# Optimization experiments

Hardware: AMD Instinct MI355X
Metric: run time of the kernel (lower is better)

Reference implementation:

```python
import jax, jax.numpy as jnp
import numpy as np

N_NODES = 50000
N_EDGES = 200000
D = 128
LN_EPS = 1e-5


def _layer_norm(x, g, b):
    mu = jnp.mean(x, axis=-1, keepdims=True)
    var = jnp.mean(jnp.square(x - mu), axis=-1, keepdims=True)
    return (x - mu) * jax.lax.rsqrt(var + LN_EPS) * g + b


def _mlp(x, W1, b1, W2, b2, W3, b3, g, beta):
    # 2 hidden ReLU layers + linear output + LayerNorm (MeshGraphNets style)
    h = jax.nn.relu(x @ W1 + b1)
    h = jax.nn.relu(h @ W2 + b2)
    h = h @ W3 + b3
    return _layer_norm(h, g, beta)


def setup_inputs() -> dict:
    key = jax.random.key(0)
    ks = jax.random.split(key, 12)
    d = {}
    d["node_features"] = jax.random.normal(ks[0], (N_NODES, D), dtype=jnp.float32)
    d["edge_features"] = jax.random.normal(ks[1], (N_EDGES, D), dtype=jnp.float32)
    d["senders"] = jax.random.randint(ks[2], (N_EDGES,), 0, N_NODES, dtype=jnp.int32)
    d["receivers"] = jax.random.randint(ks[3], (N_EDGES,), 0, N_NODES, dtype=jnp.int32)
    def lin(k, fan_in, fan_out):
        return jax.random.normal(k, (fan_in, fan_out), dtype=jnp.float32) / np.sqrt(fan_in)
    # edge MLP: [3D] -> D -> D -> D
    d["We1"] = lin(ks[4], 3 * D, D); d["be1"] = jnp.zeros((D,), jnp.float32)
    d["We2"] = lin(ks[5], D, D);     d["be2"] = jnp.zeros((D,), jnp.float32)
    d["We3"] = lin(ks[6], D, D);     d["be3"] = jnp.zeros((D,), jnp.float32)
    d["ge"] = jnp.ones((D,), jnp.float32); d["bege"] = jnp.zeros((D,), jnp.float32)
    # node MLP: [2D] -> D -> D -> D
    d["Wn1"] = lin(ks[7], 2 * D, D); d["bn1"] = jnp.zeros((D,), jnp.float32)
    d["Wn2"] = lin(ks[8], D, D);     d["bn2"] = jnp.zeros((D,), jnp.float32)
    d["Wn3"] = lin(ks[9], D, D);     d["bn3"] = jnp.zeros((D,), jnp.float32)
    d["gn"] = jnp.ones((D,), jnp.float32); d["begn"] = jnp.zeros((D,), jnp.float32)
    return d


def reference(node_features, edge_features, senders, receivers,
              We1, be1, We2, be2, We3, be3, ge, bege,
              Wn1, bn1, Wn2, bn2, Wn3, bn3, gn, begn):
    num_nodes = node_features.shape[0]
    # --- edge update: gather sender/receiver feats, concat, edge MLP ---
    edge_in = jnp.concatenate(
        [node_features[senders], node_features[receivers], edge_features], axis=-1)  # [E, 3D]
    new_edge = _mlp(edge_in, We1, be1, We2, be2, We3, be3, ge, bege)  # [E, D]
    # --- node update: scatter-sum aggregate, concat, node MLP ---
    agg = jax.ops.segment_sum(new_edge, receivers, num_segments=num_nodes)  # [N, D]
    node_in = jnp.concatenate([node_features, agg], axis=-1)  # [N, 2D]
    new_node = _mlp(node_in, Wn1, bn1, Wn2, bn2, Wn3, bn3, gn, begn)
    # --- residuals ---
    new_node = new_node + node_features
    new_edge = new_edge + edge_features
    return new_node, new_edge
```

## Files before the change

kernel.cpp:

```cpp
#include <hip/hip_runtime.h>

#define NNODES 50000
#define NEDGES 200000
#define DD 128
#define LN_EPS 1e-5f
#define NTH 256

typedef __attribute__((ext_vector_type(8))) short bf16x8;
typedef __attribute__((ext_vector_type(4))) float f32x4;
typedef __attribute__((ext_vector_type(16))) float f32x16;

template<int N> struct ic { static constexpr int value = N; };

__device__ __forceinline__ unsigned short bfr(float f) {
    union { float f; unsigned u; } v; v.f = f;
    return (unsigned short)((v.u + 0x7fffu + ((v.u >> 16) & 1u)) >> 16);
}
__device__ __forceinline__ unsigned pk2(float a, float b) {
    return (unsigned)bfr(a) | ((unsigned)bfr(b) << 16);
}
__device__ __forceinline__ void gload_lds16(const void* g, void* l) {
    __builtin_amdgcn_global_load_lds(
        (const __attribute__((address_space(1))) void*)g,
        (__attribute__((address_space(3))) void*)l, 16, 0, 0);
}

__global__ void build_wimg(const float* __restrict__ We1, const float* __restrict__ We2,
                           const float* __restrict__ We3, const float* __restrict__ Wn1,
                           const float* __restrict__ Wn2, const float* __restrict__ Wn3,
                           char* __restrict__ img_e, char* __restrict__ img_n) {
    int tid = blockIdx.x * NTH + threadIdx.x;
    const float* W; char* dst; int q;
    if      (tid <  6144) { W = We1; dst = img_e;             q = tid;         }
    else if (tid <  8192) { W = We2; dst = img_e + 12 * 8192; q = tid - 6144;  }
    else if (tid < 10240) { W = We3; dst = img_e + 16 * 8192; q = tid - 8192;  }
    else if (tid < 14336) { W = Wn1; dst = img_n;             q = tid - 10240; }
    else if (tid < 16384) { W = Wn2; dst = img_n + 8 * 8192;  q = tid - 14336; }
    else if (tid < 18432) { W = Wn3; dst = img_n + 12 * 8192; q = tid - 16384; }
    else return;
    int c = q >> 9, rem = q & 511;
    int nt = rem >> 7, r2 = rem & 127, n32 = r2 >> 2, ks = r2 & 3;
    int n = nt * 32 + n32;
    int sx = (n32 + (n32 >> 2)) & 3;
    int k0 = c * 32 + ks * 8;
    unsigned short o[8];
    #pragma unroll
    for (int e = 0; e < 8; ++e)
        o[e] = bfr(W[(size_t)(k0 + e) * DD + n]);
    uint4 val;
    val.x = (unsigned)o[0] | ((unsigned)o[1] << 16);
    val.y = (unsigned)o[2] | ((unsigned)o[3] << 16);
    val.z = (unsigned)o[4] | ((unsigned)o[5] << 16);
    val.w = (unsigned)o[6] | ((unsigned)o[7] << 16);
    *(uint4*)(dst + (size_t)c * 8192 + nt * 2048 + n32 * 64 + ((ks ^ sx) << 4)) = val;
}

__global__ __launch_bounds__(NTH)
void cvt_histo(const float* __restrict__ nodef, const int* __restrict__ recv,
               uint4* __restrict__ nodb, int* __restrict__ cnt) {
    const int tid0 = blockIdx.x * NTH + threadIdx.x;
    if (tid0 < NEDGES) atomicAdd(&cnt[recv[tid0]], 1);
    const int NG = NNODES * 16;
    for (int g = tid0; g < NG; g += gridDim.x * NTH) {
        f32x4 a = ((const f32x4*)nodef)[g * 2];
        f32x4 b = ((const f32x4*)nodef)[g * 2 + 1];
        uint4 o;
        o.x = pk2(a[0], a[1]); o.y = pk2(a[2], a[3]);
        o.z = pk2(b[0], b[1]); o.w = pk2(b[2], b[3]);
        nodb[g] = o;
    }
}

__global__ __launch_bounds__(NTH)
void csr_scan1(const int* __restrict__ cnt, int* __restrict__ part) {
    __shared__ int red[NTH];
    const int b = blockIdx.x, t = threadIdx.x;
    const int base = b * 196;
    int s = 0;
    for (int i = t; i < 196; i += NTH) {
        int idx = base + i;
        if (idx < NNODES) s += cnt[idx];
    }
    red[t] = s;
    __syncthreads();
    for (int d = NTH / 2; d > 0; d >>= 1) {
        if (t < d) red[t] += red[t + d];
        __syncthreads();
    }
    if (t == 0) part[b] = red[0];
}

__global__ __launch_bounds__(NTH)
void csr_scan2(const int* __restrict__ cnt, const int* __restrict__ part,
               int* __restrict__ off, int* __restrict__ cursor) {
    __shared__ int sp[NTH];
    const int t = threadIdx.x;
    sp[t] = part[t];
    __syncthreads();
    for (int d = 1; d < NTH; d <<= 1) {
        int v = (t >= d) ? sp[t - d] : 0;
        __syncthreads();
        sp[t] += v;
        __syncthreads();
    }
    int run = (t == 0) ? 0 : sp[t - 1];
    const int base = t * 196;
    for (int i = 0; i < 196; ++i) {
        int idx = base + i;
        if (idx < NNODES) { off[idx] = run; cursor[idx] = run; run += cnt[idx]; }
    }
    if (t == NTH - 1) off[NNODES] = NEDGES;
}

__global__ void csr_fill(const int* __restrict__ recv, int* __restrict__ cursor,
                         int* __restrict__ elist) {
    int e = blockIdx.x * NTH + threadIdx.x;
    if (e < NEDGES) {
        int p = atomicAdd(&cursor[recv[e]], 1);
        elist[p] = e;
    }
}

__global__ __launch_bounds__(NTH)
void aggregate(const unsigned* __restrict__ ybuf,
               const int* __restrict__ off, const int* __restrict__ elist,
               unsigned* __restrict__ aggb) {
    const int n = blockIdx.x * 4 + (threadIdx.x >> 6);
    const int l = threadIdx.x & 63;
    if (n >= NNODES) return;
    const int j0 = off[n], j1 = off[n + 1];
    float sx = 0.f, sy = 0.f;
    int j = j0;
    for (; j + 4 <= j1; j += 4) {
        unsigned v0 = ybuf[(size_t)elist[j] * 64 + l];
        unsigned v1 = ybuf[(size_t)elist[j + 1] * 64 + l];
        unsigned v2 = ybuf[(size_t)elist[j + 2] * 64 + l];
        unsigned v3 = ybuf[(size_t)elist[j + 3] * 64 + l];
        sx += __uint_as_float(v0 << 16) + __uint_as_float(v1 << 16)
            + __uint_as_float(v2 << 16) + __uint_as_float(v3 << 16);
        sy += __uint_as_float(v0 & 0xffff0000u) + __uint_as_float(v1 & 0xffff0000u)
            + __uint_as_float(v2 & 0xffff0000u) + __uint_as_float(v3 & 0xffff0000u);
    }
    for (; j < j1; ++j) {
        unsigned v = ybuf[(size_t)elist[j] * 64 + l];
        sx += __uint_as_float(v << 16);
        sy += __uint_as_float(v & 0xffff0000u);
    }
    aggb[(size_t)n * 64 + l] = pk2(sx, sy);
}

template<int MODE>
__global__ __launch_bounds__(NTH, 2)
void mgn_mfma(const float* __restrict__ nodef, const float* __restrict__ edgef,
              const unsigned short* __restrict__ nodb,
              const int* __restrict__ senders, const int* __restrict__ receivers,
              const char* __restrict__ img,
              const float* __restrict__ b1, const float* __restrict__ b2,
              const float* __restrict__ b3,
              const float* __restrict__ gamma, const float* __restrict__ beta,
              const unsigned short* __restrict__ aggb, unsigned* __restrict__ ybuf,
              float* __restrict__ outp)
{
    __shared__ char Wbuf[5 * 8192];
    __shared__ char Hb[4 * 8192];

    const int t  = threadIdx.x;
    const int w  = t >> 6;
    const int l  = t & 63;
    const int ln = l & 31;
    const int hi = l >> 5;
    const int row0 = blockIdx.x * 128;
    const int gm = row0 + w * 32 + ln;
    constexpr int NROWS = (MODE == 0) ? NEDGES : NNODES;
    constexpr int NK1   = (MODE == 0) ? 12 : 8;
    constexpr int NCH   = NK1 + 8;
    const int gmc = gm < NROWS ? gm : NROWS - 1;
    const int sxA = (ln + (ln >> 2)) & 3;
    const int sxH = ln & 15;

    int srow = 0, rrow = 0;
    if (MODE == 0) { srow = senders[gmc]; rrow = receivers[gmc]; }

    const f32x16 fz = {0.f,0.f,0.f,0.f,0.f,0.f,0.f,0.f,
                       0.f,0.f,0.f,0.f,0.f,0.f,0.f,0.f};
    f32x16 acc[4];
    #pragma unroll
    for (int nt = 0; nt < 4; ++nt) acc[nt] = fz;

    bf16x8 bS[3][2];
    f32x4  fS[3][4];

    auto stageW = [&](int c) {
        const char* src = img + (size_t)c * 8192 + t * 16;
        char* dstl = Wbuf + (c % 5) * 8192 + t * 16;
        gload_lds16(src, dstl);
        gload_lds16(src + 4096, dstl + 4096);
    };

    auto loadBB = [&](auto CC, bf16x8* dst) {
        constexpr int c = decltype(CC)::value;
        const unsigned short* base;
        if constexpr (MODE == 0) {
            base = (c < 4) ? nodb + (size_t)srow * DD : nodb + (size_t)rrow * DD;
        } else {
            base = (c < 4) ? nodb + (size_t)gmc * DD : aggb + (size_t)gmc * DD;
        }
        const char* p = (const char*)base + (c & 3) * 64 + hi * 16;
        dst[0] = *(const bf16x8*)p;
        dst[1] = *(const bf16x8*)(p + 32);
    };

    auto loadBF = [&](auto CC, f32x4* dst) {
        constexpr int c = decltype(CC)::value;
        const float* p = edgef + (size_t)gmc * DD + (c & 3) * 32 + hi * 8;
        dst[0] = *(const f32x4*)p;
        dst[1] = *(const f32x4*)(p + 4);
        dst[2] = *(const f32x4*)(p + 16);
        dst[3] = *(const f32x4*)(p + 20);
    };

    auto cvtB = [&](const f32x4* br) {
        union { unsigned u[4]; bf16x8 v; } r;
        r.u[0] = pk2(br[0][0], br[0][1]);
        r.u[1] = pk2(br[0][2], br[0][3]);
        r.u[2] = pk2(br[1][0], br[1][1]);
        r.u[3] = pk2(br[1][2], br[1][3]);
        return r.v;
    };

    auto loadBH = [&](int ks, int kh) {
        const char* p = Hb + w * 8192 + ln * 256
                      + (((ks * 4 + kh * 2 + hi) ^ sxH) << 4);
        return *(const bf16x8*)p;
    };

    auto getB = [&](auto CC, int kh) -> bf16x8 {
        constexpr int c = decltype(CC)::value;
        if constexpr (c >= NK1) {
            return loadBH((c - NK1) & 3, kh);
        } else if constexpr (MODE == 0 && c >= 8) {
            return cvtB(&fS[c % 3][kh * 2]);
        } else {
            return bS[c % 3][kh];
        }
    };

    auto compute = [&](auto CC) {
        constexpr int c = decltype(CC)::value;
        const char* bp = Wbuf + (c % 5) * 8192 + ln * 64;
        #pragma unroll
        for (int kh = 0; kh < 2; ++kh) {
            bf16x8 b = getB(CC, kh);
            #pragma unroll
            for (int nt = 0; nt < 4; ++nt) {
                bf16x8 a = *(const bf16x8*)(bp + nt * 2048
                            + (((kh * 2 + hi) ^ sxA) << 4));
                acc[nt] = __builtin_amdgcn_mfma_f32_32x32x16_bf16(a, b, acc[nt], 0, 0, 0);
            }
        }
    };

    auto epiH = [&](const float* bias) {
        #pragma unroll
        for (int nt = 0; nt < 4; ++nt) {
            #pragma unroll
            for (int rq = 0; rq < 4; ++rq) {
                f32x4 bv = *(const f32x4*)(bias + nt * 32 + rq * 8 + hi * 4);
                unsigned short h[4];
                #pragma unroll
                for (int j = 0; j < 4; ++j)
                    h[j] = bfr(fmaxf(acc[nt][rq * 4 + j] + bv[j], 0.f));
                char* p = Hb + w * 8192 + ln * 256
                        + (((nt * 4 + rq) ^ sxH) << 4) + hi * 8;
                unsigned lo = (unsigned)h[0] | ((unsigned)h[1] << 16);
                unsigned hx = (unsigned)h[2] | ((unsigned)h[3] << 16);
                *(unsigned long long*)p =
                    (unsigned long long)lo | ((unsigned long long)hx << 32);
            }
            acc[nt] = fz;
        }
    };

#define PITER(C, VM)                                                          \
    {                                                                         \
        if constexpr ((C) + 3 < NCH) stageW((C) + 3);                         \
        __builtin_amdgcn_sched_barrier(0);                                    \
        if constexpr ((C) + 2 < NK1) {                                        \
            if constexpr (MODE == 0 && (C) + 2 >= 8)                          \
                loadBF(ic<(C) + 2>{}, fS[((C) + 2) % 3]);                     \
            else                                                              \
                loadBB(ic<(C) + 2>{}, bS[((C) + 2) % 3]);                     \
        }                                                                     \
        __builtin_amdgcn_sched_barrier(0);                                    \
        asm volatile("s_waitcnt vmcnt(" #VM ")" ::: "memory");                \
        __builtin_amdgcn_sched_barrier(0);                                    \
        __builtin_amdgcn_s_barrier();                                         \
        __builtin_amdgcn_sched_barrier(0);                                    \
        compute(ic<(C)>{});                                                   \
    }

    stageW(0);
    __builtin_amdgcn_sched_barrier(0);
    loadBB(ic<0>{}, bS[0]);
    __builtin_amdgcn_sched_barrier(0);
    stageW(1);
    __builtin_amdgcn_sched_barrier(0);
    loadBB(ic<1>{}, bS[1]);
    __builtin_amdgcn_sched_barrier(0);
    stageW(2);
    __builtin_amdgcn_sched_barrier(0);

    if constexpr (MODE == 0) {
        PITER(0, 10)  PITER(1, 10)  PITER(2, 10)  PITER(3, 12)
        PITER(4, 12)  PITER(5, 12)  PITER(6, 14)  PITER(7, 16)
        PITER(8, 18)  PITER(9, 20)  PITER(10, 16) PITER(11, 12)
        epiH(b1);
        PITER(12, 8)  PITER(13, 4)  PITER(14, 4)  PITER(15, 4)
        epiH(b2);
        PITER(16, 4)  PITER(17, 2)  PITER(18, 0)  PITER(19, 0)
    } else {
        PITER(0, 10)  PITER(1, 10)  PITER(2, 10)  PITER(3, 12)
        PITER(4, 12)  PITER(5, 12)  PITER(6, 10)  PITER(7, 8)
        epiH(b1);
        PITER(8, 6)   PITER(9, 4)   PITER(10, 4)  PITER(11, 4)
        epiH(b2);
        PITER(12, 4)  PITER(13, 2)  PITER(14, 0)  PITER(15, 0)
    }
#undef PITER

    float vsum = 0.f, vsq = 0.f;
    #pragma unroll
    for (int nt = 0; nt < 4; ++nt) {
        #pragma unroll
        for (int rq = 0; rq < 4; ++rq) {
            f32x4 bv = *(const f32x4*)(b3 + nt * 32 + rq * 8 + hi * 4);
            #pragma unroll
            for (int j = 0; j < 4; ++j) {
                float v = acc[nt][rq * 4 + j] + bv[j];
                acc[nt][rq * 4 + j] = v;
                vsum += v; vsq += v * v;
            }
        }
    }
    vsum += __shfl_xor(vsum, 32);
    vsq  += __shfl_xor(vsq, 32);
    const float mu = vsum * (1.f / DD);
    const float rs = rsqrtf(vsq * (1.f / DD) - mu * mu + LN_EPS);

    if (gm < NROWS) {
        const float* resid = ((MODE == 0) ? edgef : nodef) + (size_t)gm * DD;
        #pragma unroll
        for (int nt = 0; nt < 4; ++nt) {
            #pragma unroll
            for (int rq = 0; rq < 4; ++rq) {
                const int n0 = nt * 32 + rq * 8 + hi * 4;
                f32x4 gv = *(const f32x4*)(gamma + n0);
                f32x4 bv = *(const f32x4*)(beta + n0);
                f32x4 rv = *(const f32x4*)(resid + n0);
                float y[4];
                f32x4 o;
                #pragma unroll
                for (int j = 0; j < 4; ++j) {
                    y[j] = (acc[nt][rq * 4 + j] - mu) * rs * gv[j] + bv[j];
                    o[j] = y[j] + rv[j];
                }
                *(f32x4*)(outp + (size_t)gm * DD + n0) = o;
                if (MODE == 0) {
                    unsigned long long pkd =
                        (unsigned long long)pk2(y[0], y[1])
                      | ((unsigned long long)pk2(y[2], y[3]) << 32);
                    *(unsigned long long*)((char*)ybuf + (size_t)gm * 256 + n0 * 2) = pkd;
                }
            }
        }
    }
}

extern "C" void kernel_launch(void* const* d_in, const int* in_sizes, int n_in,
                              void* d_out, int out_size, void* d_ws, size_t ws_size,
                              hipStream_t stream) {
    const float* nodef = (const float*)d_in[0];
    const float* edgef = (const float*)d_in[1];
    const int* senders   = (const int*)d_in[2];
    const int* receivers = (const int*)d_in[3];
    const float* We1 = (const float*)d_in[4],  *be1 = (const float*)d_in[5];
    const float* We2 = (const float*)d_in[6],  *be2 = (const float*)d_in[7];
    const float* We3 = (const float*)d_in[8],  *be3 = (const float*)d_in[9];
    const float* ge  = (const float*)d_in[10], *bege = (const float*)d_in[11];
    const float* Wn1 = (const float*)d_in[12], *bn1 = (const float*)d_in[13];
    const float* Wn2 = (const float*)d_in[14], *bn2 = (const float*)d_in[15];
    const float* Wn3 = (const float*)d_in[16], *bn3 = (const float*)d_in[17];
    const float* gn  = (const float*)d_in[18], *begn = (const float*)d_in[19];

    float* out_node = (float*)d_out;
    float* out_edge = (float*)d_out + (size_t)NNODES * DD;

    char* ws = (char*)d_ws;
    size_t o = 0;
    unsigned short* aggb = (unsigned short*)(ws + o); o += (size_t)NNODES * 256;
    unsigned* ybuf = (unsigned*)(ws + o);             o += (size_t)NEDGES * 256;
    unsigned short* nodb = (unsigned short*)(ws + o); o += (size_t)NNODES * 256;
    char* img_e = ws + o;           o += 20 * 8192;
    char* img_n = ws + o;           o += 16 * 8192;
    int* cnt    = (int*)(ws + o);   o += NNODES * 4;
    int* cursor = (int*)(ws + o);   o += NNODES * 4;
    int* off    = (int*)(ws + o);   o += (NNODES + 4) * 4;
    int* part   = (int*)(ws + o);   o += NTH * 4;
    int* elist  = (int*)(ws + o);   o += NEDGES * 4;

    hipMemsetAsync(cnt, 0, NNODES * 4, stream);
    cvt_histo<<<1024, NTH, 0, stream>>>(nodef, receivers, (uint4*)nodb, cnt);
    build_wimg<<<72, NTH, 0, stream>>>(We1, We2, We3, Wn1, Wn2, Wn3, img_e, img_n);
    csr_scan1<<<NTH, NTH, 0, stream>>>(cnt, part);
    csr_scan2<<<1, NTH, 0, stream>>>(cnt, part, off, cursor);
    csr_fill<<<(NEDGES + NTH - 1) / NTH, NTH, 0, stream>>>(receivers, cursor, elist);

    mgn_mfma<0><<<dim3((NEDGES + 127) / 128), dim3(NTH), 0, stream>>>(
        nodef, edgef, nodb, senders, receivers, img_e,
        be1, be2, be3, ge, bege, aggb, ybuf, out_edge);

    aggregate<<<(NNODES + 3) / 4, NTH, 0, stream>>>(ybuf, off, elist, (unsigned*)aggb);

    mgn_mfma<1><<<dim3((NNODES + 127) / 128), dim3(NTH), 0, stream>>>(
        nodef, edgef, nodb, senders, receivers, img_n,
        bn1, bn2, bn3, gn, begn, aggb, ybuf, out_node);
}
```

Before: 321.3 us.

## Scatter bf16 edge outputs into receiver-sorted order so aggregation reads contiguously

The CSR fill now records each edge's slot position (perm) rather than a list of edge ids. The edge MLP kernel writes its bf16 copy of each edge result directly into that receiver-sorted slot, so the aggregate kernel reads contiguous rows without the elist indirection. This trades a gathered read in aggregation for scattered 8-byte writes in the edge kernel. The PITER scheduling constants are also retuned.

```diff
diff --git a/kernel.cpp b/kernel.cpp
--- a/kernel.cpp
+++ b/kernel.cpp
@@ -113,17 +113,17 @@
 }
 
 __global__ void csr_fill(const int* __restrict__ recv, int* __restrict__ cursor,
-                         int* __restrict__ elist) {
+                         int* __restrict__ perm) {
     int e = blockIdx.x * NTH + threadIdx.x;
     if (e < NEDGES) {
         int p = atomicAdd(&cursor[recv[e]], 1);
-        elist[p] = e;
+        perm[e] = p;
     }
 }
 
 __global__ __launch_bounds__(NTH)
 void aggregate(const unsigned* __restrict__ ybuf,
-               const int* __restrict__ off, const int* __restrict__ elist,
+               const int* __restrict__ off,
                unsigned* __restrict__ aggb) {
     const int n = blockIdx.x * 4 + (threadIdx.x >> 6);
     const int l = threadIdx.x & 63;
@@ -132,17 +132,17 @@
     float sx = 0.f, sy = 0.f;
     int j = j0;
     for (; j + 4 <= j1; j += 4) {
-        unsigned v0 = ybuf[(size_t)elist[j] * 64 + l];
-        unsigned v1 = ybuf[(size_t)elist[j + 1] * 64 + l];
-        unsigned v2 = ybuf[(size_t)elist[j + 2] * 64 + l];
-        unsigned v3 = ybuf[(size_t)elist[j + 3] * 64 + l];
+        unsigned v0 = ybuf[(size_t)j * 64 + l];
+        unsigned v1 = ybuf[(size_t)(j + 1) * 64 + l];
+        unsigned v2 = ybuf[(size_t)(j + 2) * 64 + l];
+        unsigned v3 = ybuf[(size_t)(j + 3) * 64 + l];
         sx += __uint_as_float(v0 << 16) + __uint_as_float(v1 << 16)
             + __uint_as_float(v2 << 16) + __uint_as_float(v3 << 16);
         sy += __uint_as_float(v0 & 0xffff0000u) + __uint_as_float(v1 & 0xffff0000u)
             + __uint_as_float(v2 & 0xffff0000u) + __uint_as_float(v3 & 0xffff0000u);
     }
     for (; j < j1; ++j) {
-        unsigned v = ybuf[(size_t)elist[j] * 64 + l];
+        unsigned v = ybuf[(size_t)j * 64 + l];
         sx += __uint_as_float(v << 16);
         sy += __uint_as_float(v & 0xffff0000u);
     }
@@ -154,6 +154,7 @@
 void mgn_mfma(const float* __restrict__ nodef, const float* __restrict__ edgef,
               const unsigned short* __restrict__ nodb,
               const int* __restrict__ senders, const int* __restrict__ receivers,
+              const int* __restrict__ perm,
               const char* __restrict__ img,
               const float* __restrict__ b1, const float* __restrict__ b2,
               const float* __restrict__ b3,
@@ -178,8 +179,8 @@
     const int sxA = (ln + (ln >> 2)) & 3;
     const int sxH = ln & 15;
 
-    int srow = 0, rrow = 0;
-    if (MODE == 0) { srow = senders[gmc]; rrow = receivers[gmc]; }
+    int srow = 0, rrow = 0, prow = 0;
+    if (MODE == 0) { srow = senders[gmc]; rrow = receivers[gmc]; prow = perm[gmc]; }
 
     const f32x16 fz = {0.f,0.f,0.f,0.f,0.f,0.f,0.f,0.f,
                        0.f,0.f,0.f,0.f,0.f,0.f,0.f,0.f};
@@ -311,20 +312,20 @@
     __builtin_amdgcn_sched_barrier(0);
 
     if constexpr (MODE == 0) {
-        PITER(0, 10)  PITER(1, 10)  PITER(2, 10)  PITER(3, 12)
-        PITER(4, 12)  PITER(5, 12)  PITER(6, 14)  PITER(7, 16)
-        PITER(8, 18)  PITER(9, 20)  PITER(10, 16) PITER(11, 12)
+        PITER(0, 12)  PITER(1, 12)  PITER(2, 12)  PITER(3, 14)
+        PITER(4, 14)  PITER(5, 14)  PITER(6, 14)  PITER(7, 14)
+        PITER(8, 14)  PITER(9, 14)  PITER(10, 12) PITER(11, 10)
         epiH(b1);
-        PITER(12, 8)  PITER(13, 4)  PITER(14, 4)  PITER(15, 4)
+        PITER(12, 8)  PITER(13, 6)  PITER(14, 6)  PITER(15, 6)
         epiH(b2);
-        PITER(16, 4)  PITER(17, 2)  PITER(18, 0)  PITER(19, 0)
+        PITER(16, 6)  PITER(17, 4)  PITER(18, 2)  PITER(19, 0)
     } else {
-        PITER(0, 10)  PITER(1, 10)  PITER(2, 10)  PITER(3, 12)
-        PITER(4, 12)  PITER(5, 12)  PITER(6, 10)  PITER(7, 8)
+        PITER(0, 12)  PITER(1, 12)  PITER(2, 12)  PITER(3, 14)
+        PITER(4, 14)  PITER(5, 14)  PITER(6, 12)  PITER(7, 10)
         epiH(b1);
-        PITER(8, 6)   PITER(9, 4)   PITER(10, 4)  PITER(11, 4)
+        PITER(8, 8)   PITER(9, 6)   PITER(10, 6)  PITER(11, 6)
         epiH(b2);
-        PITER(12, 4)  PITER(13, 2)  PITER(14, 0)  PITER(15, 0)
+        PITER(12, 6)  PITER(13, 4)  PITER(14, 2)  PITER(15, 0)
     }
 #undef PITER
 
@@ -369,7 +370,7 @@
                     unsigned long long pkd =
                         (unsigned long long)pk2(y[0], y[1])
                       | ((unsigned long long)pk2(y[2], y[3]) << 32);
-                    *(unsigned long long*)((char*)ybuf + (size_t)gm * 256 + n0 * 2) = pkd;
+                    *(unsigned long long*)((char*)ybuf + (size_t)prow * 256 + n0 * 2) = pkd;
                 }
             }
         }
@@ -406,22 +407,22 @@
     int* cursor = (int*)(ws + o);   o += NNODES * 4;
     int* off    = (int*)(ws + o);   o += (NNODES + 4) * 4;
     int* part   = (int*)(ws + o);   o += NTH * 4;
-    int* elist  = (int*)(ws + o);   o += NEDGES * 4;
+    int* perm   = (int*)(ws + o);   o += NEDGES * 4;
 
     hipMemsetAsync(cnt, 0, NNODES * 4, stream);
     cvt_histo<<<1024, NTH, 0, stream>>>(nodef, receivers, (uint4*)nodb, cnt);
     build_wimg<<<72, NTH, 0, stream>>>(We1, We2, We3, Wn1, Wn2, Wn3, img_e, img_n);
     csr_scan1<<<NTH, NTH, 0, stream>>>(cnt, part);
     csr_scan2<<<1, NTH, 0, stream>>>(cnt, part, off, cursor);
-    csr_fill<<<(NEDGES + NTH - 1) / NTH, NTH, 0, stream>>>(receivers, cursor, elist);
+    csr_fill<<<(NEDGES + NTH - 1) / NTH, NTH, 0, stream>>>(receivers, cursor, perm);
 
     mgn_mfma<0><<<dim3((NEDGES + 127) / 128), dim3(NTH), 0, stream>>>(
-        nodef, edgef, nodb, senders, receivers, img_e,
+        nodef, edgef, nodb, senders, receivers, perm, img_e,
         be1, be2, be3, ge, bege, aggb, ybuf, out_edge);
 
-    aggregate<<<(NNODES + 3) / 4, NTH, 0, stream>>>(ybuf, off, elist, (unsigned*)aggb);
+    aggregate<<<(NNODES + 3) / 4, NTH, 0, stream>>>(ybuf, off, (unsigned*)aggb);
 
     mgn_mfma<1><<<dim3((NNODES + 127) / 128), dim3(NTH), 0, stream>>>(
-        nodef, edgef, nodb, senders, receivers, img_n,
+        nodef, edgef, nodb, senders, receivers, perm, img_n,
         bn1, bn2, bn3, gn, begn, aggb, ybuf, out_node);
 }
```

Result: no change. 316.3 us (-1.5%).
